# Kernel tuning notes

Measured on AMD Instinct MI355X. Metric: run time of the kernel, lower is better.

## Reference

```python
import jax, jax.numpy as jnp
import numpy as np

N_EMBD = 2560
N_HEAD = 32
HEAD_DIM = N_EMBD // N_HEAD  # 80
ROTARY_DIM = 32
SEQ = 2048
BSZ = 1


def _rope_tables(seq_len, rotary_dim, base=10000.0):
    inv_freq = 1.0 / (base ** (np.arange(0, rotary_dim, 2, dtype=np.float32) / rotary_dim))
    t = np.arange(seq_len, dtype=np.float32)
    freqs = np.outer(t, inv_freq)                      # [S, rd/2]
    emb = np.concatenate([freqs, freqs], axis=-1)      # [S, rd]
    return jnp.asarray(np.cos(emb)), jnp.asarray(np.sin(emb))


def setup_inputs() -> dict:
    key = jax.random.key(0)
    k1, k2, k3, k4, k5 = jax.random.split(key, 5)
    op_size = HEAD_DIM * (N_HEAD + 2 * N_HEAD)  # fused q,k,v => 3*n_embd
    hidden_states = jax.random.normal(k1, (BSZ, SEQ, N_EMBD), dtype=jnp.float32)
    Wqkv_w = jax.random.normal(k2, (op_size, N_EMBD), dtype=jnp.float32) * 0.02
    Wqkv_b = jax.random.normal(k3, (op_size,), dtype=jnp.float32) * 0.02
    out_w = jax.random.normal(k4, (N_EMBD, N_EMBD), dtype=jnp.float32) * 0.02
    out_b = jax.random.normal(k5, (N_EMBD,), dtype=jnp.float32) * 0.02
    cos, sin = _rope_tables(SEQ, ROTARY_DIM)
    return {"hidden_states": hidden_states, "Wqkv_w": Wqkv_w, "Wqkv_b": Wqkv_b,
            "out_w": out_w, "out_b": out_b, "cos": cos, "sin": sin}


def apply_partial_rotary(x, cos, sin):
    # x: [S, B, H, D]; cos/sin: [S, rd]
    rd = cos.shape[-1]
    c = cos[:, None, None, :]
    s = sin[:, None, None, :]
    x_rot = x[..., :rd]
    # NOTE: faithful to source -- rotated half is concatenated WITHOUT negation
    tmp = jnp.concatenate([x[..., rd // 2:rd], x[..., :rd // 2]], axis=-1)
    rotten = x_rot * c + tmp * s
    return jnp.concatenate([rotten, x[..., rd:]], axis=-1)


def reference(hidden_states, Wqkv_w, Wqkv_b, out_w, out_b, cos, sin):
    bsz, q_len, _ = hidden_states.shape
    qkv = hidden_states @ Wqkv_w.T + Wqkv_b            # [B, S, 3*E]
    q, k, v = jnp.split(qkv, 3, axis=-1)
    # [B, S, H, D] -> [S, B, H, D] for rotary
    q = q.reshape(bsz, q_len, N_HEAD, HEAD_DIM).transpose(1, 0, 2, 3)
    k = k.reshape(bsz, q_len, N_HEAD, HEAD_DIM).transpose(1, 0, 2, 3)
    v = v.reshape(bsz, q_len, N_HEAD, HEAD_DIM).transpose(0, 2, 1, 3)  # [B, H, S, D]
    cos_t, sin_t = cos[:q_len], sin[:q_len]
    q = apply_partial_rotary(q, cos_t, sin_t).transpose(1, 2, 0, 3)    # [B, H, S, D]
    k = apply_partial_rotary(k, cos_t, sin_t).transpose(1, 2, 0, 3)    # [B, H, S, D]
    scale = 1.0 / jnp.sqrt(jnp.asarray(HEAD_DIM, dtype=q.dtype))
    scores = jnp.einsum('bhqd,bhkd->bhqk', q, k) * scale
    causal = jnp.tril(jnp.ones((q_len, q_len), dtype=bool))
    scores = jnp.where(causal, scores, jnp.asarray(-1e30, dtype=scores.dtype))
    probs = jax.nn.softmax(scores, axis=-1)
    out = jnp.einsum('bhqk,bhkd->bhqd', probs, v)       # [B, H, S, D]
    out = out.transpose(0, 2, 1, 3).reshape(bsz, q_len, N_EMBD)
    return out @ out_w.T + out_b
```

## Files before the change

kernel.cpp:

```cpp
#include <hip/hip_runtime.h>
#include <cstdint>
#include <cstddef>

typedef unsigned short bf16_t;
typedef __attribute__((ext_vector_type(8))) short bf16x8;
typedef __attribute__((ext_vector_type(4))) float f32x4;

__device__ __forceinline__ float bf2f(bf16_t b) {
  unsigned int u = ((unsigned int)b) << 16;
  return __builtin_bit_cast(float, u);
}
__device__ __forceinline__ bf16_t f2bf(float f) {
  unsigned int u = __builtin_bit_cast(unsigned int, f);
  u += 0x7fffu + ((u >> 16) & 1u);
  return (bf16_t)(u >> 16);
}
__device__ __forceinline__ float exp2_hw(float x) {
  return __builtin_amdgcn_exp2f(x);
}

constexpr int SEQ = 2048, NE = 2560, NH = 32, HD = 80, OP = 7680;

__global__ void cvt3(const float* __restrict__ s0, const float* __restrict__ s1,
                     const float* __restrict__ s2, bf16_t* __restrict__ d0,
                     bf16_t* __restrict__ d1, bf16_t* __restrict__ d2)
{
  constexpr int N0 = SEQ * NE / 4, N1 = OP * NE / 4;
  int t = blockIdx.x * 256 + threadIdx.x;
  const float* s; bf16_t* d;
  if (t < N0)            { s = s0; d = d0; }
  else if (t < N0 + N1)  { s = s1; d = d1; t -= N0; }
  else                   { s = s2; d = d2; t -= N0 + N1; }
  float4 v = ((const float4*)s)[t];
  ushort4 o;
  o.x = f2bf(v.x); o.y = f2bf(v.y); o.z = f2bf(v.z); o.w = f2bf(v.w);
  ((ushort4*)d)[t] = o;
}

__device__ __forceinline__ void store_out(bf16_t* p, float v) { *p = f2bf(v); }
__device__ __forceinline__ void store_out(float* p, float v)  { *p = v; }

template <typename OutT>
__global__ __launch_bounds__(256, 2) void gemm_bt_bias(
    const bf16_t* __restrict__ A,
    const bf16_t* __restrict__ B,
    const float*  __restrict__ bias,
    OutT* __restrict__ C,
    int M, int N, int K, int klen)
{
  __shared__ bf16_t As[2][128 * 32];
  __shared__ bf16_t Bs[2][128 * 32];

  const int tid  = threadIdx.x;
  const int lane = tid & 63;
  const int wave = tid >> 6;
  const int m0 = blockIdx.y * 128;
  const int n0 = blockIdx.x * 128;
  const int kbeg = blockIdx.z * klen;
  OutT* Cz = C + (size_t)blockIdx.z * M * N;
  const int mw = (wave >> 1) * 64;
  const int nw = (wave & 1) * 64;
  const int lm = lane & 15;
  const int lq = lane >> 4;

  f32x4 acc[4][4];
#pragma unroll
  for (int i = 0; i < 4; ++i)
#pragma unroll
    for (int j = 0; j < 4; ++j)
      acc[i][j] = (f32x4){0.f, 0.f, 0.f, 0.f};

  const int ldr = lane >> 2;
  const int ldc = (lane & 3) * 8;

  for (int kt = kbeg; kt < kbeg + klen; kt += 64) {
#pragma unroll
    for (int sub = 0; sub < 2; ++sub) {
#pragma unroll
      for (int r = 0; r < 2; ++r) {
        const int seg = wave * 2 + r;
        const int row = seg * 16 + ldr;
        const int col = kt + sub * 32 + ldc;
        const bf16_t* ga = A + (size_t)(m0 + row) * K + col;
        const bf16_t* gb = B + (size_t)(n0 + row) * K + col;
        __builtin_amdgcn_global_load_lds(
            (const __attribute__((address_space(1))) unsigned int*)ga,
            (__attribute__((address_space(3))) unsigned int*)&As[sub][seg * 512], 16, 0, 0);
        __builtin_amdgcn_global_load_lds(
            (const __attribute__((address_space(1))) unsigned int*)gb,
            (__attribute__((address_space(3))) unsigned int*)&Bs[sub][seg * 512], 16, 0, 0);
      }
    }
    __syncthreads();

#pragma unroll
    for (int sub = 0; sub < 2; ++sub) {
      bf16x8 af[4], bfq[4];
#pragma unroll
      for (int i = 0; i < 4; ++i)
        af[i] = *(const bf16x8*)&As[sub][(mw + i * 16 + lm) * 32 + lq * 8];
#pragma unroll
      for (int j = 0; j < 4; ++j)
        bfq[j] = *(const bf16x8*)&Bs[sub][(nw + j * 16 + lm) * 32 + lq * 8];

#pragma unroll
      for (int i = 0; i < 4; ++i)
#pragma unroll
        for (int j = 0; j < 4; ++j)
          acc[i][j] = __builtin_amdgcn_mfma_f32_16x16x32_bf16(af[i], bfq[j], acc[i][j], 0, 0, 0);
    }

    __syncthreads();
  }

#pragma unroll
  for (int i = 0; i < 4; ++i) {
#pragma unroll
    for (int j = 0; j < 4; ++j) {
      const int n = n0 + nw + j * 16 + lm;
      const float bv = bias ? bias[n] : 0.f;
#pragma unroll
      for (int r = 0; r < 4; ++r) {
        const int m = m0 + mw + i * 16 + lq * 4 + r;
        store_out(&Cz[(size_t)m * N + n], acc[i][j][r] + bv);
      }
    }
  }
}

__global__ void reduce2_bias(const float* __restrict__ p, const float* __restrict__ bias,
                             float* __restrict__ out)
{
  const int t = blockIdx.x * 256 + threadIdx.x;
  const float4 a = ((const float4*)p)[t];
  const float4 b = ((const float4*)(p + (size_t)SEQ * NE))[t];
  const float4 bv = ((const float4*)bias)[t % (NE / 4)];
  float4 r;
  r.x = a.x + b.x + bv.x; r.y = a.y + b.y + bv.y;
  r.z = a.z + b.z + bv.z; r.w = a.w + b.w + bv.w;
  ((float4*)out)[t] = r;
}

__global__ void rope_kernel(bf16_t* __restrict__ qkv,
                            const float* __restrict__ cosb,
                            const float* __restrict__ sinb)
{
  const int t = blockIdx.x * 256 + threadIdx.x;
  const int i  = t & 15;
  const int qk = (t >> 4) & 1;
  const int h  = (t >> 5) & 31;
  const int s  = t >> 10;
  const size_t base = (size_t)s * OP + qk * NE + h * HD;
  const float xi = bf2f(qkv[base + i]);
  const float xj = bf2f(qkv[base + i + 16]);
  const float c1 = cosb[s * 32 + i];
  const float s1 = sinb[s * 32 + i];
  const float c2 = cosb[s * 32 + i + 16];
  const float s2 = sinb[s * 32 + i + 16];
  qkv[base + i]      = f2bf(xi * c1 + xj * s1);
  qkv[base + i + 16] = f2bf(xj * c2 + xi * s2);
}

constexpr int TSTR = 82;
__global__ void vtrans(const bf16_t* __restrict__ qkv, bf16_t* __restrict__ vtg)
{
  __shared__ bf16_t T[64 * TSTR];
  const int h  = blockIdx.y;
  const int sb = blockIdx.x * 64;
  const int tid = threadIdx.x;
  const int voff = 2 * NE + h * HD;

#pragma unroll
  for (int i = 0; i < 10; ++i) {
    const int u = i * 256 + tid;
    const int row = u / 40, c = u % 40;
    const unsigned int w = *(const unsigned int*)(qkv + (size_t)(sb + row) * OP + voff + 2 * c);
    *(unsigned int*)&T[row * TSTR + 2 * c] = w;
  }
  __syncthreads();

  bf16_t* vh = vtg + (size_t)h * HD * SEQ;
#pragma unroll
  for (int i = 0; i < 10; ++i) {
    const int u = i * 256 + tid;
    const int d = u >> 5, sp = u & 31;
    const unsigned int lo = T[(2 * sp) * TSTR + d];
    const unsigned int hi = T[(2 * sp + 1) * TSTR + d];
    *(unsigned int*)(vh + (size_t)d * SEQ + sb + 2 * sp) = lo | (hi << 16);
  }
}

constexpr int KSTR = 96;
constexpr int VSTR = 72;
constexpr int PSTR = 72;

__global__ __launch_bounds__(256, 4) void attn_mfma(
    const bf16_t* __restrict__ qkv, const bf16_t* __restrict__ vtg,
    bf16_t* __restrict__ aout)
{
  __shared__ bf16_t Ks[12 * 512];
  __shared__ bf16_t Vt[12 * 512];
  __shared__ bf16_t Ps[4][16 * PSTR];

  const int h    = blockIdx.y;
  const int qt   = (int)gridDim.x - 1 - blockIdx.x;
  const int q0   = qt * 64;
  const int tid  = threadIdx.x;
  const int lane = tid & 63;
  const int wave = tid >> 6;
  const int lm   = lane & 15;
  const int quad = lane >> 4;

  const int qg = q0 + 16 * wave + lm;

  const int koff = NE + h * HD;
  const bf16_t* vh = vtg + (size_t)h * HD * SEQ;
  const float EC = 0.1118033988749895f * 1.4426950408889634f;

  bf16x8 qf[3];
  {
    const bf16_t* q_r = qkv + (size_t)qg * OP + h * HD;
#pragma unroll
    for (int ks = 0; ks < 3; ++ks) {
      const int col = ks * 32 + quad * 8;
      if (col < 80) qf[ks] = *(const bf16x8*)(q_r + col);
      else          qf[ks] = (bf16x8){0,0,0,0,0,0,0,0};
    }
  }

  int kofs[3];
#pragma unroll
  for (int r = 0; r < 3; ++r) {
    const int e = (wave * 3 + r) * 512 + lane * 8;
    const int row = e / 96, c = e % 96;
    kofs[r] = row * OP + (c < 80 ? c : c - 16);
  }
  int vofs[3];
#pragma unroll
  for (int r = 0; r < 3; ++r) {
    const int e = (wave * 3 + r) * 512 + lane * 8;
    int row = e / 72;
    const int c = e % 72;
    if (row >= 80) row -= 80;
    vofs[r] = row * SEQ + (c < 64 ? c : c - 16);
  }

  f32x4 oacc[5];
#pragma unroll
  for (int mt = 0; mt < 5; ++mt) oacc[mt] = (f32x4){0.f,0.f,0.f,0.f};
  float lsum = 0.f;

  const int ntiles = qt + 1;
  for (int t = 0; t < ntiles; ++t) {
    const int kb = t * 64;

#pragma unroll
    for (int r = 0; r < 3; ++r) {
      const bf16_t* gk = qkv + (size_t)kb * OP + koff + kofs[r];
      __builtin_amdgcn_global_load_lds(
          (const __attribute__((address_space(1))) unsigned int*)gk,
          (__attribute__((address_space(3))) unsigned int*)&Ks[(wave * 3 + r) * 512],
          16, 0, 0);
      const bf16_t* gv = vh + kb + vofs[r];
      __builtin_amdgcn_global_load_lds(
          (const __attribute__((address_space(1))) unsigned int*)gv,
          (__attribute__((address_space(3))) unsigned int*)&Vt[(wave * 3 + r) * 512],
          16, 0, 0);
    }
    __syncthreads();

    f32x4 sacc[4];
#pragma unroll
    for (int mt = 0; mt < 4; ++mt) sacc[mt] = (f32x4){0.f,0.f,0.f,0.f};
#pragma unroll
    for (int ks = 0; ks < 3; ++ks) {
      bf16x8 kf[4];
#pragma unroll
      for (int mt = 0; mt < 4; ++mt)
        kf[mt] = *(const bf16x8*)&Ks[(mt * 16 + lm) * KSTR + ks * 32 + quad * 8];
#pragma unroll
      for (int mt = 0; mt < 4; ++mt)
        sacc[mt] = __builtin_amdgcn_mfma_f32_16x16x32_bf16(kf[mt], qf[ks], sacc[mt], 0, 0, 0);
    }

    if (t == ntiles - 1) {
      const int keyb = kb + quad * 4;
#pragma unroll
      for (int mt = 0; mt < 4; ++mt) {
        float ps[4];
#pragma unroll
        for (int r = 0; r < 4; ++r) {
          float p = exp2_hw(sacc[mt][r] * EC);
          p = (keyb + mt * 16 + r > qg) ? 0.f : p;
          ps[r] = p;
        }
        lsum += (ps[0] + ps[1]) + (ps[2] + ps[3]);
        ushort4 pk;
        pk.x = f2bf(ps[0]); pk.y = f2bf(ps[1]); pk.z = f2bf(ps[2]); pk.w = f2bf(ps[3]);
        *(ushort4*)&Ps[wave][lm * PSTR + mt * 16 + quad * 4] = pk;
      }
    } else {
#pragma unroll
      for (int mt = 0; mt < 4; ++mt) {
        float ps[4];
#pragma unroll
        for (int r = 0; r < 4; ++r) ps[r] = exp2_hw(sacc[mt][r] * EC);
        lsum += (ps[0] + ps[1]) + (ps[2] + ps[3]);
        ushort4 pk;
        pk.x = f2bf(ps[0]); pk.y = f2bf(ps[1]); pk.z = f2bf(ps[2]); pk.w = f2bf(ps[3]);
        *(ushort4*)&Ps[wave][lm * PSTR + mt * 16 + quad * 4] = pk;
      }
    }

#pragma unroll
    for (int ks = 0; ks < 2; ++ks) {
      bf16x8 vf[5], pf;
#pragma unroll
      for (int mt = 0; mt < 5; ++mt)
        vf[mt] = *(const bf16x8*)&Vt[(mt * 16 + lm) * VSTR + ks * 32 + quad * 8];
      pf = *(const bf16x8*)&Ps[wave][lm * PSTR + ks * 32 + quad * 8];
#pragma unroll
      for (int mt = 0; mt < 5; ++mt)
        oacc[mt] = __builtin_amdgcn_mfma_f32_16x16x32_bf16(vf[mt], pf, oacc[mt], 0, 0, 0);
    }
    __syncthreads();
  }

  lsum += __shfl_xor(lsum, 16);
  lsum += __shfl_xor(lsum, 32);
  const float inv = 1.f / lsum;
  bf16_t* base = aout + (size_t)qg * NE + h * HD + quad * 4;
#pragma unroll
  for (int mt = 0; mt < 5; ++mt) {
    ushort4 st;
    st.x = f2bf(oacc[mt][0] * inv);
    st.y = f2bf(oacc[mt][1] * inv);
    st.z = f2bf(oacc[mt][2] * inv);
    st.w = f2bf(oacc[mt][3] * inv);
    *(ushort4*)(base + mt * 16) = st;
  }
}

extern "C" void kernel_launch(void* const* d_in, const int* in_sizes, int n_in,
                              void* d_out, int out_size, void* d_ws, size_t ws_size,
                              hipStream_t stream)
{
  const float* hs   = (const float*)d_in[0];
  const float* wqkv = (const float*)d_in[1];
  const float* bqkv = (const float*)d_in[2];
  const float* wout = (const float*)d_in[3];
  const float* bout = (const float*)d_in[4];
  const float* cosb = (const float*)d_in[5];
  const float* sinb = (const float*)d_in[6];

  bf16_t* hs_bf   = (bf16_t*)d_ws;
  bf16_t* wqkv_bf = hs_bf   + (size_t)SEQ * NE;
  bf16_t* wout_bf = wqkv_bf + (size_t)OP * NE;
  bf16_t* qkv     = wout_bf + (size_t)NE * NE;
  bf16_t* aout    = qkv     + (size_t)SEQ * OP;
  float*  out     = (float*)d_out;
  bf16_t* vtg     = hs_bf;
  float*  pbuf    = (float*)d_ws;

  constexpr int CVT_T = (SEQ * NE + OP * NE + NE * NE) / 4;
  cvt3<<<CVT_T / 256, 256, 0, stream>>>(hs, wqkv, wout, hs_bf, wqkv_bf, wout_bf);

  gemm_bt_bias<bf16_t><<<dim3(OP / 128, SEQ / 128, 1), 256, 0, stream>>>(
      hs_bf, wqkv_bf, bqkv, qkv, SEQ, OP, NE, NE);
  rope_kernel<<<(SEQ * NH * 2 * 16) / 256, 256, 0, stream>>>(qkv, cosb, sinb);
  vtrans<<<dim3(SEQ / 64, NH), 256, 0, stream>>>(qkv, vtg);
  attn_mfma<<<dim3(SEQ / 64, NH), 256, 0, stream>>>(qkv, vtg, aout);
  gemm_bt_bias<float><<<dim3(NE / 128, SEQ / 128, 2), 256, 0, stream>>>(
      aout, wout_bf, nullptr, pbuf, SEQ, NE, NE, NE / 2);
  reduce2_bias<<<(SEQ * NE / 4) / 256, 256, 0, stream>>>(pbuf, bout, out);
}
```

Measured before the change: 412.0 us.

## Add 256x256-tile QKV GEMM with direct-to-LDS loads and staged pipelining

Adds a new QKV projection GEMM kernel that uses 256x256 output tiles, 512 threads and a K-step of 64. Operand tiles are loaded straight into swizzled LDS with global_load_lds and double-buffered. The loads are interleaved with four MFMA phases, each fenced by barriers and raised wave priority. The goal is more data reuse per tile and better overlap of memory with MFMA work. The cost is a much larger LDS footprint and heavy register use for accumulators. The grid also shrinks to 30x8 = 240 blocks, which may underfill the GPU.

```diff
diff --git a/kernel.cpp b/kernel.cpp
--- a/kernel.cpp
+++ b/kernel.cpp
@@ -39,6 +39,164 @@
 
 __device__ __forceinline__ void store_out(bf16_t* p, float v) { *p = f2bf(v); }
 __device__ __forceinline__ void store_out(float* p, float v)  { *p = v; }
+
+__global__ __launch_bounds__(512, 2) void gemm256_bt_bias(
+    const bf16_t* __restrict__ A,
+    const bf16_t* __restrict__ B,
+    const float*  __restrict__ bias,
+    bf16_t* __restrict__ C,
+    int M, int N, int K)
+{
+  __shared__ bf16_t As[2][256 * 64];
+  __shared__ bf16_t Bs[2][256 * 64];
+
+  const int tid  = threadIdx.x;
+  const int lane = tid & 63;
+  const int wave = tid >> 6;
+  const int wm   = wave >> 2;
+  const int wn   = wave & 3;
+  const int lm   = lane & 15;
+  const int quad = lane >> 4;
+  const int m0 = blockIdx.y * 256;
+  const int n0 = blockIdx.x * 256;
+  const int NT = K / 64;
+
+  const int srow = lane >> 3;
+  const int scol = ((lane & 7) ^ srow) * 8;
+
+  auto stage = [&](const bf16_t* __restrict__ P, int R0, int K0, int H, bf16_t* DST) {
+#pragma unroll
+    for (int cc = 0; cc < 2; ++cc) {
+      const int seg = wave * 2 + cc;
+      const bf16_t* src = P + (size_t)(R0 + H * 128 + seg * 8 + srow) * K + K0 + scol;
+      __builtin_amdgcn_global_load_lds(
+          (const __attribute__((address_space(1))) unsigned int*)src,
+          (__attribute__((address_space(3))) unsigned int*)(DST + H * 8192 + seg * 512),
+          16, 0, 0);
+    }
+  };
+
+  const int xk0 = ((0 + quad) ^ (lm & 7)) * 8;
+  const int xk1 = ((4 + quad) ^ (lm & 7)) * 8;
+
+  f32x4 acc[8][4];
+#pragma unroll
+  for (int i = 0; i < 8; ++i)
+#pragma unroll
+    for (int j = 0; j < 4; ++j)
+      acc[i][j] = (f32x4){0.f, 0.f, 0.f, 0.f};
+
+  stage(A, m0, 0, 0, As[0]);  stage(A, m0, 0, 1, As[0]);
+  stage(B, n0, 0, 0, Bs[0]);  stage(B, n0, 0, 1, Bs[0]);
+  stage(A, m0, 64, 0, As[1]); stage(A, m0, 64, 1, As[1]);
+
+  for (int t = 0; t < NT; ++t) {
+    const int c = t & 1;
+    bf16_t* Asn = As[c ^ 1];
+    bf16_t* Bsn = Bs[c ^ 1];
+    const bf16_t* Ab = &As[c][(wm * 128 + lm) * 64];
+    const bf16_t* Bb = &Bs[c][(wn * 64 + lm) * 64];
+
+    if (t == NT - 1) asm volatile("s_waitcnt vmcnt(0)" ::: "memory");
+    else             asm volatile("s_waitcnt vmcnt(4)" ::: "memory");
+    __builtin_amdgcn_s_barrier();
+
+    bf16x8 a[4][2], b01[2][2], b23[2][2];
+
+#pragma unroll
+    for (int i = 0; i < 4; ++i) {
+      a[i][0] = *(const bf16x8*)(Ab + i * 1024 + xk0);
+      a[i][1] = *(const bf16x8*)(Ab + i * 1024 + xk1);
+    }
+#pragma unroll
+    for (int j = 0; j < 2; ++j) {
+      b01[j][0] = *(const bf16x8*)(Bb + j * 1024 + xk0);
+      b01[j][1] = *(const bf16x8*)(Bb + j * 1024 + xk1);
+    }
+    if (t + 1 < NT) stage(B, n0, (t + 1) * 64, 0, Bsn);
+    __builtin_amdgcn_s_barrier();
+    asm volatile("s_waitcnt lgkmcnt(0)" ::: "memory");
+    __builtin_amdgcn_sched_barrier(0);
+    __builtin_amdgcn_s_setprio(1);
+#pragma unroll
+    for (int kk = 0; kk < 2; ++kk)
+#pragma unroll
+      for (int i = 0; i < 4; ++i)
+#pragma unroll
+        for (int j = 0; j < 2; ++j)
+          acc[i][j] = __builtin_amdgcn_mfma_f32_16x16x32_bf16(a[i][kk], b01[j][kk], acc[i][j], 0, 0, 0);
+    __builtin_amdgcn_s_setprio(0);
+    __builtin_amdgcn_s_barrier();
+
+#pragma unroll
+    for (int j = 0; j < 2; ++j) {
+      b23[j][0] = *(const bf16x8*)(Bb + (2 + j) * 1024 + xk0);
+      b23[j][1] = *(const bf16x8*)(Bb + (2 + j) * 1024 + xk1);
+    }
+    if (t + 1 < NT) stage(B, n0, (t + 1) * 64, 1, Bsn);
+    __builtin_amdgcn_s_barrier();
+    asm volatile("s_waitcnt lgkmcnt(0)" ::: "memory");
+    __builtin_amdgcn_sched_barrier(0);
+    __builtin_amdgcn_s_setprio(1);
+#pragma unroll
+    for (int kk = 0; kk < 2; ++kk)
+#pragma unroll
+      for (int i = 0; i < 4; ++i)
+#pragma unroll
+        for (int j = 0; j < 2; ++j)
+          acc[i][2 + j] = __builtin_amdgcn_mfma_f32_16x16x32_bf16(a[i][kk], b23[j][kk], acc[i][2 + j], 0, 0, 0);
+    __builtin_amdgcn_s_setprio(0);
+    __builtin_amdgcn_s_barrier();
+
+#pragma unroll
+    for (int i = 0; i < 4; ++i) {
+      a[i][0] = *(const bf16x8*)(Ab + (4 + i) * 1024 + xk0);
+      a[i][1] = *(const bf16x8*)(Ab + (4 + i) * 1024 + xk1);
+    }
+    __builtin_amdgcn_s_barrier();
+    asm volatile("s_waitcnt lgkmcnt(0)" ::: "memory");
+    __builtin_amdgcn_sched_barrier(0);
+    __builtin_amdgcn_s_setprio(1);
+#pragma unroll
+    for (int kk = 0; kk < 2; ++kk)
+#pragma unroll
+      for (int i = 0; i < 4; ++i)
+#pragma unroll
+        for (int j = 0; j < 2; ++j)
+          acc[4 + i][j] = __builtin_amdgcn_mfma_f32_16x16x32_bf16(a[i][kk], b01[j][kk], acc[4 + i][j], 0, 0, 0);
+    __builtin_amdgcn_s_setprio(0);
+    __builtin_amdgcn_s_barrier();
+
+    if (t + 2 < NT) {
+      stage(A, m0, (t + 2) * 64, 0, (bf16_t*)As[c]);
+      stage(A, m0, (t + 2) * 64, 1, (bf16_t*)As[c]);
+    }
+    __builtin_amdgcn_s_barrier();
+    __builtin_amdgcn_s_setprio(1);
+#pragma unroll
+    for (int kk = 0; kk < 2; ++kk)
+#pragma unroll
+      for (int i = 0; i < 4; ++i)
+#pragma unroll
+        for (int j = 0; j < 2; ++j)
+          acc[4 + i][2 + j] = __builtin_amdgcn_mfma_f32_16x16x32_bf16(a[i][kk], b23[j][kk], acc[4 + i][2 + j], 0, 0, 0);
+    __builtin_amdgcn_s_setprio(0);
+  }
+
+#pragma unroll
+  for (int i = 0; i < 8; ++i) {
+#pragma unroll
+    for (int j = 0; j < 4; ++j) {
+      const int n = n0 + wn * 64 + j * 16 + lm;
+      const float bv = bias ? bias[n] : 0.f;
+#pragma unroll
+      for (int r = 0; r < 4; ++r) {
+        const int m = m0 + wm * 128 + i * 16 + quad * 4 + r;
+        C[(size_t)m * N + n] = f2bf(acc[i][j][r] + bv);
+      }
+    }
+  }
+}
 
 template <typename OutT>
 __global__ __launch_bounds__(256, 2) void gemm_bt_bias(
@@ -365,8 +523,8 @@
   constexpr int CVT_T = (SEQ * NE + OP * NE + NE * NE) / 4;
   cvt3<<<CVT_T / 256, 256, 0, stream>>>(hs, wqkv, wout, hs_bf, wqkv_bf, wout_bf);
 
-  gemm_bt_bias<bf16_t><<<dim3(OP / 128, SEQ / 128, 1), 256, 0, stream>>>(
-      hs_bf, wqkv_bf, bqkv, qkv, SEQ, OP, NE, NE);
+  gemm256_bt_bias<<<dim3(OP / 256, SEQ / 256), 512, 0, stream>>>(
+      hs_bf, wqkv_bf, bqkv, qkv, SEQ, OP, NE);
   rope_kernel<<<(SEQ * NH * 2 * 16) / 256, 256, 0, stream>>>(qkv, cosb, sinb);
   vtrans<<<dim3(SEQ / 64, NH), 256, 0, stream>>>(qkv, vtg);
   attn_mfma<<<dim3(SEQ / 64, NH), 256, 0, stream>>>(qkv, vtg, aout);
```

Measured after the change: 393.5 us. 4.5% less time.
